# Optimization experiments

Measured on AMD Instinct MI355X. Metric: run time of the kernel, lower is better.

Reference implementation:

```python
import jax, jax.numpy as jnp
import numpy as np

NUM_HEADS = 8
NUM_LEVELS = 4
NUM_POINTS = 4
EMBED = 256
BS = 8
NQ = 900
SPATIAL = np.array([[92, 160], [46, 80], [23, 40], [12, 20]], dtype=np.int64)  # (h, w) per level
NV = int((SPATIAL[:, 0] * SPATIAL[:, 1]).sum())  # 19560


def setup_inputs() -> dict:
    key = jax.random.key(0)
    ks = jax.random.split(key, 12)
    s = 0.02
    return {
        'query': jax.random.normal(ks[0], (BS, NQ, EMBED), jnp.float32),
        'value': jax.random.normal(ks[1], (BS, NV, EMBED), jnp.float32),
        'reference_points': jax.random.uniform(ks[2], (BS, NQ, NUM_LEVELS, 2), jnp.float32),
        'Wv': jax.random.normal(ks[3], (EMBED, EMBED), jnp.float32) * s,
        'bv': jnp.zeros((EMBED,), jnp.float32),
        'Ws': jax.random.normal(ks[4], (EMBED, NUM_HEADS * NUM_LEVELS * NUM_POINTS * 2), jnp.float32) * s,
        'bs_off': jax.random.normal(ks[5], (NUM_HEADS * NUM_LEVELS * NUM_POINTS * 2,), jnp.float32) * 0.5,
        'Wa': jax.random.normal(ks[6], (EMBED, NUM_HEADS * NUM_LEVELS * NUM_POINTS), jnp.float32) * s,
        'ba': jnp.zeros((NUM_HEADS * NUM_LEVELS * NUM_POINTS,), jnp.float32),
        'Wo': jax.random.normal(ks[7], (EMBED, EMBED), jnp.float32) * s,
        'bo': jnp.zeros((EMBED,), jnp.float32),
        'spatial_shapes': jnp.asarray(SPATIAL),
    }


def _gather(vflat, idx):
    # vflat: (B, H, N, dh); idx: (B, H, M) int32 -> (B, H, M, dh)
    return jnp.take_along_axis(vflat, idx[..., None], axis=2)


def _bilinear(vflat, x, y, Hl, Wl):
    # vflat: (B, H, Hl*Wl, dh); x, y: (B, H, M) pixel coords (align_corners=False, zero padding)
    x0 = jnp.floor(x); y0 = jnp.floor(y)
    wx1 = x - x0; wx0 = 1.0 - wx1
    wy1 = y - y0; wy0 = 1.0 - wy1
    acc = 0.0
    for xi, yi, w in ((x0, y0, wx0 * wy0), (x0 + 1, y0, wx1 * wy0),
                      (x0, y0 + 1, wx0 * wy1), (x0 + 1, y0 + 1, wx1 * wy1)):
        valid = (xi >= 0) & (xi < Wl) & (yi >= 0) & (yi < Hl)
        xc = jnp.clip(xi, 0, Wl - 1).astype(jnp.int32)
        yc = jnp.clip(yi, 0, Hl - 1).astype(jnp.int32)
        v = _gather(vflat, yc * Wl + xc)
        acc = acc + v * (w * valid)[..., None]
    return acc  # (B, H, M, dh)


def reference(query, value, reference_points, Wv, bv, Ws, bs_off, Wa, ba, Wo, bo, spatial_shapes):
    B, Q, E = query.shape
    H, L, P = NUM_HEADS, NUM_LEVELS, NUM_POINTS
    dh = E // H
    shapes = np.asarray(spatial_shapes)  # static (L, 2) (h, w)

    v = value @ Wv + bv                              # (B, NV, E)
    v = v.reshape(B, -1, H, dh)                      # (B, NV, H, dh)

    off = (query @ Ws + bs_off).reshape(B, Q, H, L, P, 2)
    attn = jax.nn.softmax((query @ Wa + ba).reshape(B, Q, H, L * P), axis=-1)
    attn = attn.reshape(B, Q, H, L, P)

    norm = jnp.asarray(shapes[:, ::-1].copy(), jnp.float32)  # (L, 2) = (w, h)
    loc = reference_points[:, :, None, :, None, :] + off / norm[None, None, None, :, None, :]
    # loc: (B, Q, H, L, P, 2) normalized in [0, 1]

    out = jnp.zeros((B, H, Q, dh), query.dtype)
    start = 0
    for l in range(L):
        Hl, Wl = int(shapes[l, 0]), int(shapes[l, 1])
        vl = v[:, start:start + Hl * Wl].transpose(0, 2, 1, 3)  # (B, H, Hl*Wl, dh)
        start += Hl * Wl
        # grid_sample align_corners=False pixel coords
        x = loc[:, :, :, l, :, 0] * Wl - 0.5                     # (B, Q, H, P)
        y = loc[:, :, :, l, :, 1] * Hl - 0.5
        x = x.transpose(0, 2, 1, 3).reshape(B, H, Q * P)
        y = y.transpose(0, 2, 1, 3).reshape(B, H, Q * P)
        samp = _bilinear(vl, x, y, Hl, Wl).reshape(B, H, Q, P, dh)
        w_l = attn[:, :, :, l, :].transpose(0, 2, 1, 3)          # (B, H, Q, P)
        out = out + (samp * w_l[..., None]).sum(axis=3)
    out = out.transpose(0, 2, 1, 3).reshape(B, Q, E)
    out = out @ Wo + bo
    return out + query  # identity residual (dropout=0 at inference)
```

## Files before the change

kernel.cpp:

```cpp
#include <hip/hip_runtime.h>
#include <hip/hip_bf16.h>


#define B_   8
#define NQ_  900
#define E_   256
#define H_   8
#define NV_  19560
#define M_TOT (B_ * NV_)
#define MQ_  (B_ * NQ_)
#define NVB  2445
#define NPB  225

typedef __attribute__((ext_vector_type(8)))  __bf16 bf16x8;
typedef __attribute__((ext_vector_type(4)))  float  f32x4;
typedef __attribute__((ext_vector_type(16))) float  f32x16;

__device__ __forceinline__ unsigned short f2bf(float x) {
    unsigned int u = __builtin_bit_cast(unsigned int, x);
    u += 0x7FFFu + ((u >> 16) & 1u);
    return (unsigned short)(u >> 16);
}

__device__ __forceinline__ unsigned int pack2bf(float a, float b) {
    union { __hip_bfloat162 h; unsigned int u; } r;
    r.h = __float22bfloat162_rn(make_float2(a, b));
    return r.u;
}

__device__ __forceinline__ bf16x8 cvt8(f32x4 lo, f32x4 hi) {
    union { bf16x8 v; unsigned int u[4]; } r;
    r.u[0] = pack2bf(lo.x, lo.y);
    r.u[1] = pack2bf(lo.z, lo.w);
    r.u[2] = pack2bf(hi.x, hi.y);
    r.u[3] = pack2bf(hi.z, hi.w);
    return r.v;
}

__device__ __forceinline__ unsigned short bf1(float x) {
    union { __hip_bfloat16 h; unsigned short u; } r;
    r.h = __float2bfloat16(x);
    return r.u;
}

#define GLL16(src, dst) \
    __builtin_amdgcn_global_load_lds( \
        (const __attribute__((address_space(1))) unsigned int*)(src), \
        (__attribute__((address_space(3))) unsigned int*)(dst), 16, 0, 0)

__global__ __launch_bounds__(256) void k_prep(
    const float* __restrict__ Wv, const float* __restrict__ Wo,
    const float* __restrict__ Ws, const float* __restrict__ Wa,
    unsigned short* __restrict__ vimg, unsigned short* __restrict__ oimg,
    unsigned short* __restrict__ pimg)
{
    const int i = blockIdx.x * 256 + threadIdx.x;
    if (i < 131072) {
        const int e = i & 65535;
        const int j = e & 7, col = (e >> 3) & 255, h = (e >> 11) & 1, kf = e >> 12;
        const int k = kf * 16 + h * 8 + j;
        const float w = (i < 65536) ? Wv[k * 256 + col] : Wo[k * 256 + col];
        ((i < 65536) ? vimg : oimg)[e] = f2bf(w);
    } else {
        const int e = i - 131072;
        const int j = e & 7;
        const int q = e >> 3;
        const int col = q % 384, s = q / 384;
        const int h = s & 1, kf = s >> 1;
        const int k = kf * 16 + h * 8 + j;
        pimg[e] = f2bf(col < 256 ? Ws[k * 256 + col] : Wa[k * 128 + (col - 256)]);
    }
}

__device__ __forceinline__ void vg_stage(
    const float* __restrict__ value, const unsigned short* __restrict__ vimg,
    unsigned short* sA, unsigned short* sB, int row0, int ks, int t)
{
#pragma unroll
    for (int i = 0; i < 2; ++i) {
        const int u = i * 256 + t;
        const int row = u >> 3, qs = u & 7;
        const float* src = value + (long)(row0 + row) * 256 + ks * 32
                           + ((qs ^ (row & 7)) << 2);
        GLL16(src, sA + u * 8);
    }
#pragma unroll
    for (int i = 0; i < 4; ++i) {
        const int u = i * 256 + t;
        GLL16(vimg + (ks * 1024 + u) * 8, sB + u * 8);
    }
}

__device__ __forceinline__ void vg_compute(
    const unsigned short* sA, const unsigned short* sB,
    int lr, int hh, int w, f32x16 acc[2][2])
{
#pragma unroll
    for (int kk = 0; kk < 2; ++kk) {
        bf16x8 a8[2], b8[2];
#pragma unroll
        for (int m = 0; m < 2; ++m) {
            const int row = m * 32 + lr;
            const int q0 = kk * 4 + hh * 2;
            const f32x4 lo = *(const f32x4*)(sA + (row * 8 + ((q0    ) ^ (row & 7))) * 8);
            const f32x4 hi = *(const f32x4*)(sA + (row * 8 + ((q0 + 1) ^ (row & 7))) * 8);
            a8[m] = cvt8(lo, hi);
        }
#pragma unroll
        for (int n = 0; n < 2; ++n)
            b8[n] = *(const bf16x8*)(sB + ((kk * 2 + hh) * 256 + w * 64 + n * 32 + lr) * 8);
        __builtin_amdgcn_s_setprio(1);
#pragma unroll
        for (int m = 0; m < 2; ++m)
#pragma unroll
            for (int n = 0; n < 2; ++n)
                acc[m][n] = __builtin_amdgcn_mfma_f32_32x32x16_bf16(
                    a8[m], b8[n], acc[m][n], 0, 0, 0);
        __builtin_amdgcn_s_setprio(0);
    }
}

__global__ __launch_bounds__(256) void k_vparams(
    const float* __restrict__ value, const unsigned short* __restrict__ vimg,
    const float* __restrict__ bv, unsigned short* __restrict__ v_out,
    const float* __restrict__ query, const unsigned short* __restrict__ pimg,
    const float* __restrict__ bs, const float* __restrict__ ba,
    float* __restrict__ off_out, float* __restrict__ attn_out)
{
    __shared__ __attribute__((aligned(16))) unsigned short sm[24576];
    const int t = threadIdx.x, w = t >> 6, l = t & 63;
    const int lr = l & 31, hh = l >> 5;

    if (blockIdx.x < NVB) {
        unsigned short* const sA_ = sm;
        unsigned short* const sB_ = sm + 8192;
#define SA_(p) (sA_ + (p) * 4096)
#define SB_(p) (sB_ + (p) * 8192)
        const int row0 = blockIdx.x * 64;

        f32x16 acc[2][2];
#pragma unroll
        for (int m = 0; m < 2; ++m)
#pragma unroll
            for (int n = 0; n < 2; ++n) acc[m][n] = (f32x16)(0.f);

        vg_stage(value, vimg, SA_(0), SB_(0), row0, 0, t);
        vg_stage(value, vimg, SA_(1), SB_(1), row0, 1, t);

#pragma unroll
        for (int ks = 0; ks < 8; ++ks) {
            if (ks < 7) asm volatile("s_waitcnt vmcnt(6)" ::: "memory");
            else        asm volatile("s_waitcnt vmcnt(0)" ::: "memory");
            __builtin_amdgcn_sched_barrier(0);
            __builtin_amdgcn_s_barrier();
            vg_compute(SA_(ks & 1), SB_(ks & 1), lr, hh, w, acc);
            __builtin_amdgcn_s_barrier();
            __builtin_amdgcn_sched_barrier(0);
            if (ks < 6)
                vg_stage(value, vimg, SA_(ks & 1), SB_(ks & 1), row0, ks + 2, t);
        }

#pragma unroll
        for (int n = 0; n < 2; ++n) {
            const int col = w * 64 + n * 32 + lr;
            const float bb = bv[col];
#pragma unroll
            for (int m = 0; m < 2; ++m)
#pragma unroll
                for (int r = 0; r < 16; ++r) {
                    const int row = row0 + m * 32 + (r & 3) + 8 * (r >> 2) + 4 * hh;
                    v_out[(long)row * 256 + col] = bf1(acc[m][n][r] + bb);
                }
        }
    } else {
        const int row0 = (blockIdx.x - NVB) * 32;
        const float* arow = query + (long)(row0 + lr) * 256;

        f32x16 acc[3];
#pragma unroll
        for (int n = 0; n < 3; ++n) acc[n] = (f32x16)(0.f);

        f32x4 al[2], ah[2];
        al[0] = *(const f32x4*)(arow + 0 * 16 + hh * 8);
        ah[0] = *(const f32x4*)(arow + 0 * 16 + hh * 8 + 4);
        al[1] = *(const f32x4*)(arow + 1 * 16 + hh * 8);
        ah[1] = *(const f32x4*)(arow + 1 * 16 + hh * 8 + 4);

#pragma unroll
        for (int p = 0; p < 4; ++p) {
            if (p > 0) __syncthreads();
#pragma unroll
            for (int i = 0; i < 12; ++i)
                GLL16(pimg + p * 24576 + (i * 256 + t) * 8, sm + (i * 256 + t) * 8);
            __syncthreads();
#pragma unroll
            for (int kfp = 0; kfp < 4; ++kfp) {
                const int g = p * 4 + kfp;
                const int s = g & 1;
                const bf16x8 a8 = cvt8(al[s], ah[s]);
                if (g + 2 < 16) {
                    al[s] = *(const f32x4*)(arow + (g + 2) * 16 + hh * 8);
                    ah[s] = *(const f32x4*)(arow + (g + 2) * 16 + hh * 8 + 4);
                }
#pragma unroll
                for (int n = 0; n < 3; ++n) {
                    const bf16x8 b8 = *(const bf16x8*)
                        (sm + (((kfp * 2 + hh) * 384) + w * 96 + n * 32 + lr) * 8);
                    acc[n] = __builtin_amdgcn_mfma_f32_32x32x16_bf16(a8, b8, acc[n], 0, 0, 0);
                }
            }
        }

        __syncthreads();
        float* slog = (float*)sm;
#pragma unroll
        for (int n = 0; n < 3; ++n) {
            const int gcol = w * 96 + n * 32 + lr;
#pragma unroll
            for (int r = 0; r < 16; ++r) {
                const int rl = (r & 3) + 8 * (r >> 2) + 4 * hh;
                if (gcol < 256)
                    off_out[(long)(row0 + rl) * 256 + gcol] = acc[n][r] + bs[gcol];
                else
                    slog[rl * 128 + (gcol - 256)] = acc[n][r] + ba[gcol - 256];
            }
        }
        __syncthreads();
        {
            const int row = t >> 3, h = t & 7;
            const float* pl = slog + row * 128 + h * 16;
            float m = pl[0];
#pragma unroll
            for (int j = 1; j < 16; ++j) m = fmaxf(m, pl[j]);
            float e[16]; float ssum = 0.f;
#pragma unroll
            for (int j = 0; j < 16; ++j) { e[j] = expf(pl[j] - m); ssum += e[j]; }
            const float inv = 1.0f / ssum;
            float* po = attn_out + (long)(row0 + row) * 128 + h * 16;
#pragma unroll
            for (int j = 0; j < 16; ++j) po[j] = e[j] * inv;
        }
    }
}

__global__ __launch_bounds__(256) void k_sample(
    const float* __restrict__ refp, const float* __restrict__ off,
    const float* __restrict__ attn, const unsigned short* __restrict__ v,
    unsigned short* __restrict__ out_mid)
{
    __shared__ int2 spt[1024];
    const int t = threadIdx.x;
    const int img = blockIdx.x & 7, pr = blockIdx.x >> 3;
    const int bq0 = img * NQ_ + pr * 2;

    constexpr int HS[4] = {92, 46, 23, 12};
    constexpr int WS_[4] = {160, 80, 40, 20};
    constexpr int ST[4] = {0, 14720, 18400, 19320};

    {
        const int qi = t >> 7, c = t & 127;
        const int h = c >> 4, lv = (c >> 2) & 3, p = c & 3;
        const int bq = bq0 + qi;
        const int Hl = HS[lv], Wl = WS_[lv], st = ST[lv];
        const float rx = refp[bq * 8 + lv * 2 + 0];
        const float ry = refp[bq * 8 + lv * 2 + 1];
        const float ox = off[(long)bq * 256 + h * 32 + lv * 8 + p * 2 + 0];
        const float oy = off[(long)bq * 256 + h * 32 + lv * 8 + p * 2 + 1];
        const float aw = attn[(long)bq * 128 + h * 16 + lv * 4 + p];
        const float x = fmaf(rx, (float)Wl, ox) - 0.5f;
        const float y = fmaf(ry, (float)Hl, oy) - 0.5f;
        const float x0f = floorf(x), y0f = floorf(y);
        const int x0 = (int)x0f, y0 = (int)y0f;
        const float wx1 = x - x0f, wx0 = 1.f - wx1;
        const float wy1 = y - y0f, wy0 = 1.f - wy1;
#pragma unroll
        for (int cnr = 0; cnr < 4; ++cnr) {
            const int dx = cnr & 1, dy = cnr >> 1;
            const int xi = x0 + dx, yi = y0 + dy;
            const bool valid = (xi >= 0) && (xi < Wl) && (yi >= 0) && (yi < Hl);
            const int xc = min(max(xi, 0), Wl - 1);
            const int yc = min(max(yi, 0), Hl - 1);
            const float wgt = (dx ? wx1 : wx0) * (dy ? wy1 : wy0) * aw;
            spt[t * 4 + cnr] = make_int2((st + yc * Wl + xc) * 128,
                                         __builtin_bit_cast(int, valid ? wgt : 0.f));
        }
    }
    __syncthreads();

    const int qi = t >> 7, tt = t & 127;
    const int h = tt >> 4, dp = tt & 15;
    const int bq = bq0 + qi;
    const unsigned int* vb = (const unsigned int*)(v + (long)img * NV_ * 256)
                             + h * 16 + dp;
    const int2* tbl = spt + (qi * 128 + h * 16) * 4;
    float acc0 = 0.f, acc1 = 0.f;
#pragma unroll
    for (int j = 0; j < 16; ++j) {
#pragma unroll
        for (int cnr = 0; cnr < 4; ++cnr) {
            const int2 ow = tbl[j * 4 + cnr];
            const unsigned int u = vb[ow.x];
            const float wgt = __builtin_bit_cast(float, ow.y);
            acc0 = fmaf(__builtin_bit_cast(float, u << 16), wgt, acc0);
            acc1 = fmaf(__builtin_bit_cast(float, u & 0xFFFF0000u), wgt, acc1);
        }
    }
    *(unsigned int*)(out_mid + (long)bq * 256 + h * 32 + dp * 2) = pack2bf(acc0, acc1);
}

__global__ __launch_bounds__(256) void k_ogemm(
    const unsigned short* __restrict__ mid, const unsigned short* __restrict__ oimg,
    const float* __restrict__ bo, const float* __restrict__ query,
    float* __restrict__ out)
{
    __shared__ unsigned short sB[32768];
    const int t = threadIdx.x, w = t >> 6, l = t & 63;
    const int lr = l & 31, hh = l >> 5;
    const int row0 = blockIdx.x * 32;
    const unsigned short* arow = mid + (long)(row0 + lr) * 256;

    f32x16 acc[2];
#pragma unroll
    for (int n = 0; n < 2; ++n) acc[n] = (f32x16)(0.f);

    bf16x8 areg[2];
    areg[0] = *(const bf16x8*)(arow + 0 * 16 + hh * 8);
    areg[1] = *(const bf16x8*)(arow + 1 * 16 + hh * 8);

#pragma unroll
    for (int i = 0; i < 16; ++i)
        GLL16(oimg + (i * 256 + t) * 8, sB + (i * 256 + t) * 8);
    __syncthreads();

#pragma unroll
    for (int ph = 0; ph < 2; ++ph) {
        if (ph == 1) {
            __syncthreads();
#pragma unroll
            for (int i = 0; i < 16; ++i)
                GLL16(oimg + 32768 + (i * 256 + t) * 8, sB + (i * 256 + t) * 8);
            __syncthreads();
        }
#pragma unroll
        for (int kfp = 0; kfp < 8; ++kfp) {
            const int g = ph * 8 + kfp;
            const int s = g & 1;
            const bf16x8 a8 = areg[s];
            if (g + 2 < 16)
                areg[s] = *(const bf16x8*)(arow + (g + 2) * 16 + hh * 8);
#pragma unroll
            for (int n = 0; n < 2; ++n) {
                const bf16x8 b8 = *(const bf16x8*)
                    (sB + (((kfp * 2 + hh) * 256) + w * 64 + n * 32 + lr) * 8);
                acc[n] = __builtin_amdgcn_mfma_f32_32x32x16_bf16(a8, b8, acc[n], 0, 0, 0);
            }
        }
    }

#pragma unroll
    for (int n = 0; n < 2; ++n) {
        const int col = w * 64 + n * 32 + lr;
        const float bb = bo[col];
#pragma unroll
        for (int r = 0; r < 16; ++r) {
            const int row = row0 + (r & 3) + 8 * (r >> 2) + 4 * hh;
            out[(long)row * 256 + col] = acc[n][r] + bb + query[(long)row * 256 + col];
        }
    }
}

extern "C" void kernel_launch(void* const* d_in, const int* in_sizes, int n_in,
                              void* d_out, int out_size, void* d_ws, size_t ws_size,
                              hipStream_t stream)
{
    const float* query = (const float*)d_in[0];
    const float* value = (const float*)d_in[1];
    const float* refp  = (const float*)d_in[2];
    const float* Wv    = (const float*)d_in[3];
    const float* bv    = (const float*)d_in[4];
    const float* Ws    = (const float*)d_in[5];
    const float* bs    = (const float*)d_in[6];
    const float* Wa    = (const float*)d_in[7];
    const float* ba    = (const float*)d_in[8];
    const float* Wo    = (const float*)d_in[9];
    const float* bo    = (const float*)d_in[10];
    float* out = (float*)d_out;

    char* ws = (char*)d_ws;
    unsigned short* v_ws  = (unsigned short*)ws;
    float* off_ws  = (float*)(ws + 80117760);
    float* attn_ws = (float*)(ws + 87490560);
    unsigned short* mid_ws  = (unsigned short*)(ws + 91176960);
    unsigned short* vimg_ws = (unsigned short*)(ws + 94863360);
    unsigned short* pimg_ws = (unsigned short*)(ws + 94994432);
    unsigned short* oimg_ws = (unsigned short*)(ws + 95191040);

    k_prep   <<<dim3(896), dim3(256), 0, stream>>>(Wv, Wo, Ws, Wa, vimg_ws, oimg_ws, pimg_ws);
    k_vparams<<<dim3(NVB + NPB), dim3(256), 0, stream>>>(value, vimg_ws, bv, v_ws,
                                                         query, pimg_ws, bs, ba,
                                                         off_ws, attn_ws);
    k_sample <<<dim3(MQ_ / 2), dim3(256), 0, stream>>>(refp, off_ws, attn_ws, v_ws, mid_ws);
    k_ogemm  <<<dim3(MQ_ / 32), dim3(256), 0, stream>>>(mid_ws, oimg_ws, bo, query, out);
}
```

Measured before the change: 98.72 us.

## Load GEMM weight operands directly into registers, shrink LDS, raise occupancy

Both GEMM paths now read the pre-swizzled bf16 weight fragments straight from global memory into registers instead of staging them through shared memory. The value projection double-buffers the B fragments in registers, and the vmcnt waits are reordered around that. The query projection drops its staged shared-memory loop and its barriers. Shared memory shrinks from 48KB to 16KB and launch bounds request 4 blocks per CU, aiming for higher occupancy and less LDS traffic. The cost is more global/L2 reads of weights per wave and higher register pressure.

Measured after the change: 115.1 us. 16.6% more time.

```diff
diff --git a/kernel.cpp b/kernel.cpp
--- a/kernel.cpp
+++ b/kernel.cpp
@@ -72,9 +72,8 @@
     }
 }
 
-__device__ __forceinline__ void vg_stage(
-    const float* __restrict__ value, const unsigned short* __restrict__ vimg,
-    unsigned short* sA, unsigned short* sB, int row0, int ks, int t)
+__device__ __forceinline__ void vg_stageA(
+    const float* __restrict__ value, unsigned short* sA, int row0, int ks, int t)
 {
 #pragma unroll
     for (int i = 0; i < 2; ++i) {
@@ -84,20 +83,27 @@
                            + ((qs ^ (row & 7)) << 2);
         GLL16(src, sA + u * 8);
     }
-#pragma unroll
-    for (int i = 0; i < 4; ++i) {
-        const int u = i * 256 + t;
-        GLL16(vimg + (ks * 1024 + u) * 8, sB + u * 8);
-    }
+}
+
+__device__ __forceinline__ void vg_loadB(
+    const unsigned short* __restrict__ vimg, int ks, int w, int lr, int hh,
+    bf16x8 br[2][2])
+{
+#pragma unroll
+    for (int kk = 0; kk < 2; ++kk)
+#pragma unroll
+        for (int n = 0; n < 2; ++n)
+            br[kk][n] = *(const bf16x8*)
+                (vimg + (((ks * 2 + kk) * 2 + hh) * 256 + w * 64 + n * 32 + lr) * 8);
 }
 
 __device__ __forceinline__ void vg_compute(
-    const unsigned short* sA, const unsigned short* sB,
-    int lr, int hh, int w, f32x16 acc[2][2])
+    const unsigned short* sA, const bf16x8 br[2][2],
+    int lr, int hh, f32x16 acc[2][2])
 {
 #pragma unroll
     for (int kk = 0; kk < 2; ++kk) {
-        bf16x8 a8[2], b8[2];
+        bf16x8 a8[2];
 #pragma unroll
         for (int m = 0; m < 2; ++m) {
             const int row = m * 32 + lr;
@@ -106,36 +112,30 @@
             const f32x4 hi = *(const f32x4*)(sA + (row * 8 + ((q0 + 1) ^ (row & 7))) * 8);
             a8[m] = cvt8(lo, hi);
         }
-#pragma unroll
-        for (int n = 0; n < 2; ++n)
-            b8[n] = *(const bf16x8*)(sB + ((kk * 2 + hh) * 256 + w * 64 + n * 32 + lr) * 8);
         __builtin_amdgcn_s_setprio(1);
 #pragma unroll
         for (int m = 0; m < 2; ++m)
 #pragma unroll
             for (int n = 0; n < 2; ++n)
                 acc[m][n] = __builtin_amdgcn_mfma_f32_32x32x16_bf16(
-                    a8[m], b8[n], acc[m][n], 0, 0, 0);
+                    a8[m], br[kk][n], acc[m][n], 0, 0, 0);
         __builtin_amdgcn_s_setprio(0);
     }
 }
 
-__global__ __launch_bounds__(256) void k_vparams(
+__global__ __launch_bounds__(256, 4) void k_vparams(
     const float* __restrict__ value, const unsigned short* __restrict__ vimg,
     const float* __restrict__ bv, unsigned short* __restrict__ v_out,
     const float* __restrict__ query, const unsigned short* __restrict__ pimg,
     const float* __restrict__ bs, const float* __restrict__ ba,
     float* __restrict__ off_out, float* __restrict__ attn_out)
 {
-    __shared__ __attribute__((aligned(16))) unsigned short sm[24576];
+    __shared__ __attribute__((aligned(16))) unsigned short sm[8192];
     const int t = threadIdx.x, w = t >> 6, l = t & 63;
     const int lr = l & 31, hh = l >> 5;
 
     if (blockIdx.x < NVB) {
-        unsigned short* const sA_ = sm;
-        unsigned short* const sB_ = sm + 8192;
-#define SA_(p) (sA_ + (p) * 4096)
-#define SB_(p) (sB_ + (p) * 8192)
+#define SA_(p) (sm + (p) * 4096)
         const int row0 = blockIdx.x * 64;
 
         f32x16 acc[2][2];
@@ -144,20 +144,27 @@
 #pragma unroll
             for (int n = 0; n < 2; ++n) acc[m][n] = (f32x16)(0.f);
 
-        vg_stage(value, vimg, SA_(0), SB_(0), row0, 0, t);
-        vg_stage(value, vimg, SA_(1), SB_(1), row0, 1, t);
+        bf16x8 brA[2][2], brB[2][2];
+
+        vg_loadB(vimg, 0, w, lr, hh, brA);
+        vg_stageA(value, SA_(0), row0, 0, t);
+        vg_stageA(value, SA_(1), row0, 1, t);
 
 #pragma unroll
         for (int ks = 0; ks < 8; ++ks) {
+            if (ks < 7) {
+                if (ks & 1) vg_loadB(vimg, ks + 1, w, lr, hh, brA);
+                else        vg_loadB(vimg, ks + 1, w, lr, hh, brB);
+            }
             if (ks < 7) asm volatile("s_waitcnt vmcnt(6)" ::: "memory");
             else        asm volatile("s_waitcnt vmcnt(0)" ::: "memory");
             __builtin_amdgcn_sched_barrier(0);
             __builtin_amdgcn_s_barrier();
-            vg_compute(SA_(ks & 1), SB_(ks & 1), lr, hh, w, acc);
+            vg_compute(SA_(ks & 1), (ks & 1) ? brB : brA, lr, hh, acc);
             __builtin_amdgcn_s_barrier();
             __builtin_amdgcn_sched_barrier(0);
             if (ks < 6)
-                vg_stage(value, vimg, SA_(ks & 1), SB_(ks & 1), row0, ks + 2, t);
+                vg_stageA(value, SA_(ks & 1), row0, ks + 2, t);
         }
 
 #pragma unroll
@@ -187,31 +194,21 @@
         ah[1] = *(const f32x4*)(arow + 1 * 16 + hh * 8 + 4);
 
 #pragma unroll
-        for (int p = 0; p < 4; ++p) {
-            if (p > 0) __syncthreads();
-#pragma unroll
-            for (int i = 0; i < 12; ++i)
-                GLL16(pimg + p * 24576 + (i * 256 + t) * 8, sm + (i * 256 + t) * 8);
-            __syncthreads();
-#pragma unroll
-            for (int kfp = 0; kfp < 4; ++kfp) {
-                const int g = p * 4 + kfp;
-                const int s = g & 1;
-                const bf16x8 a8 = cvt8(al[s], ah[s]);
-                if (g + 2 < 16) {
-                    al[s] = *(const f32x4*)(arow + (g + 2) * 16 + hh * 8);
-                    ah[s] = *(const f32x4*)(arow + (g + 2) * 16 + hh * 8 + 4);
-                }
-#pragma unroll
-                for (int n = 0; n < 3; ++n) {
-                    const bf16x8 b8 = *(const bf16x8*)
-                        (sm + (((kfp * 2 + hh) * 384) + w * 96 + n * 32 + lr) * 8);
-                    acc[n] = __builtin_amdgcn_mfma_f32_32x32x16_bf16(a8, b8, acc[n], 0, 0, 0);
-                }
+        for (int g = 0; g < 16; ++g) {
+            const int s = g & 1;
+            const bf16x8 a8 = cvt8(al[s], ah[s]);
+            if (g + 2 < 16) {
+                al[s] = *(const f32x4*)(arow + (g + 2) * 16 + hh * 8);
+                ah[s] = *(const f32x4*)(arow + (g + 2) * 16 + hh * 8 + 4);
             }
-        }
-
-        __syncthreads();
+#pragma unroll
+            for (int n = 0; n < 3; ++n) {
+                const bf16x8 b8 = *(const bf16x8*)
+                    (pimg + ((g * 2 + hh) * 384 + w * 96 + n * 32 + lr) * 8);
+                acc[n] = __builtin_amdgcn_mfma_f32_32x32x16_bf16(a8, b8, acc[n], 0, 0, 0);
+            }
+        }
+
         float* slog = (float*)sm;
 #pragma unroll
         for (int n = 0; n < 3; ++n) {
```
